# Performance work log

Measured on AMD Instinct MI355X. Metric: run time of the kernel, lower is better.

The kernel has to match this reference:

```python
import jax, jax.numpy as jnp
import numpy as np
from jax.ops import segment_sum

N_NODES = 50000


def gcn_conv(x, src, dst, W, b, n_nodes):
    # PyG GCNConv with default add_self_loops=True, normalize=True.
    # deg includes self-loops (weight 1 each).
    deg = segment_sum(jnp.ones_like(dst, dtype=x.dtype), dst, num_segments=n_nodes) + 1.0
    dinv = jax.lax.rsqrt(deg)  # [N]
    h = x @ W                  # [N, out]
    # messages over real edges: norm[src]*norm[dst]*h[src]
    msg = h[src] * (dinv[src] * dinv[dst])[:, None]   # [E, out]
    agg = segment_sum(msg, dst, num_segments=n_nodes)  # [N, out]
    # self-loop contribution: dinv[i]^2 * h[i]
    agg = agg + h * (dinv * dinv)[:, None]
    return agg + b


def setup_inputs() -> dict:
    key = jax.random.key(0)
    k1, k2, k3, k4 = jax.random.split(key, 4)
    N, E, d_in, d_hid, d_out = N_NODES, 800000, 128, 128, 64
    x = jax.random.normal(k1, (N, d_in), dtype=jnp.float32)
    edge_index = jax.random.randint(k2, (2, E), 0, N, dtype=jnp.int64)
    W1 = jax.random.normal(k3, (d_in, d_hid), dtype=jnp.float32) / np.sqrt(d_in)
    b1 = jnp.zeros((d_hid,), dtype=jnp.float32)
    W2 = jax.random.normal(k4, (d_hid, d_out), dtype=jnp.float32) / np.sqrt(d_hid)
    b2 = jnp.zeros((d_out,), dtype=jnp.float32)
    return {"x": x, "edge_index": edge_index, "W1": W1, "b1": b1, "W2": W2, "b2": b2}


def reference(x, edge_index, W1, b1, W2, b2):
    src, dst = edge_index[0], edge_index[1]
    h = gcn_conv(x, src, dst, W1, b1, N_NODES)
    h = jax.nn.relu(h)
    out = gcn_conv(h, src, dst, W2, b2, N_NODES)
    return out
```

## Files before the change

### kernel.cpp

```cpp
#include <hip/hip_runtime.h>
#include <hip/hip_bf16.h>


#define ELL_CAP 64
#define NPART 8

typedef __attribute__((ext_vector_type(8))) short short8;
typedef __attribute__((ext_vector_type(4))) float f32x4;

static __device__ __forceinline__ unsigned short f2bf(float f) {
    unsigned int u = __float_as_uint(f);
    u = (u + 0x7fff + ((u >> 16) & 1)) >> 16;
    return (unsigned short)u;
}
static __device__ __forceinline__ float2 bfunpack(unsigned int u) {
    return make_float2(__uint_as_float(u << 16),
                       __uint_as_float(u & 0xffff0000u));
}


__global__ void init_misc(const float* __restrict__ W1, const float* __restrict__ W2,
                          short* __restrict__ w1t, short* __restrict__ w2t,
                          int* __restrict__ cnt, int n)
{
    int i = blockIdx.x * blockDim.x + threadIdx.x;
    if (i < 128 * 128) {
        int k = i >> 7, nn = i & 127;
        w1t[nn * 128 + k] = (short)f2bf(W1[i]);
    } else if (i < 128 * 128 + 128 * 64) {
        int j = i - 128 * 128;
        int k = j >> 6, nn = j & 63;
        w2t[nn * 128 + k] = (short)f2bf(W2[j]);
    }
    if (i < n) cnt[i] = 0;
}


__global__ __launch_bounds__(256) void build_ell_part(
    const int* __restrict__ src, const int* __restrict__ dst,
    int* __restrict__ cnt, unsigned short* __restrict__ ell, int E, int partSize)
{
    const int part   = blockIdx.x & (NPART - 1);
    const int chunk  = blockIdx.x >> 3;
    const int nchunk = gridDim.x >> 3;
    const int lo = part * partSize, hi = lo + partSize;

    const int  E4  = E >> 2;
    const int  per = (E4 + nchunk - 1) / nchunk;
    const int  i1  = min((chunk + 1) * per, E4);
    const int4* __restrict__ d4p = (const int4*)dst;
    const int4* __restrict__ s4p = (const int4*)src;

    for (int i = chunk * per + threadIdx.x; i < i1; i += 256) {
        int4 d4 = d4p[i];
        int4 s4 = s4p[i];
        if (d4.x >= lo && d4.x < hi) {
            int p = atomicAdd(&cnt[d4.x], 1);
            if (p < ELL_CAP) ell[(size_t)d4.x * ELL_CAP + p] = (unsigned short)s4.x;
        }
        if (d4.y >= lo && d4.y < hi) {
            int p = atomicAdd(&cnt[d4.y], 1);
            if (p < ELL_CAP) ell[(size_t)d4.y * ELL_CAP + p] = (unsigned short)s4.y;
        }
        if (d4.z >= lo && d4.z < hi) {
            int p = atomicAdd(&cnt[d4.z], 1);
            if (p < ELL_CAP) ell[(size_t)d4.z * ELL_CAP + p] = (unsigned short)s4.z;
        }
        if (d4.w >= lo && d4.w < hi) {
            int p = atomicAdd(&cnt[d4.w], 1);
            if (p < ELL_CAP) ell[(size_t)d4.w * ELL_CAP + p] = (unsigned short)s4.w;
        }
    }
    if (chunk == 0) {
        for (int e = (E & ~3) + threadIdx.x; e < E; e += 256) {
            int d = dst[e];
            if (d >= lo && d < hi) {
                int p = atomicAdd(&cnt[d], 1);
                if (p < ELL_CAP) ell[(size_t)d * ELL_CAP + p] = (unsigned short)src[e];
            }
        }
    }
}


template<int NC, bool AF32>
__global__ __launch_bounds__(256) void gemm_mfma(
    const void* __restrict__ Av, const short* __restrict__ Bt,
    const int* __restrict__ cnt, unsigned short* __restrict__ Cb, int n)
{
    __shared__ short Bs[NC][136];
    const int tid = threadIdx.x;

    #pragma unroll
    for (int i = 0; i < NC / 16; ++i) {
        int idx = tid + i * 256;
        int nrow = idx >> 4;
        int kcol = (idx & 15) * 8;
        *(short8*)&Bs[nrow][kcol] = *(const short8*)(Bt + nrow * 128 + kcol);
    }
    __syncthreads();

    const int wave = tid >> 6, lane = tid & 63;
    const int row0 = blockIdx.x * 64 + wave * 16;
    if (row0 >= n) return;
    const int quad = lane >> 4, l16 = lane & 15;

    short8 af[4];
    if (AF32) {
        const float* arow = (const float*)Av + (size_t)(row0 + l16) * 128 + quad * 8;
        #pragma unroll
        for (int kk = 0; kk < 4; ++kk) {
            float4 u = *(const float4*)(arow + kk * 32);
            float4 v = *(const float4*)(arow + kk * 32 + 4);
            short8 f;
            f[0] = (short)f2bf(u.x); f[1] = (short)f2bf(u.y);
            f[2] = (short)f2bf(u.z); f[3] = (short)f2bf(u.w);
            f[4] = (short)f2bf(v.x); f[5] = (short)f2bf(v.y);
            f[6] = (short)f2bf(v.z); f[7] = (short)f2bf(v.w);
            af[kk] = f;
        }
    } else {
        const short* arow = (const short*)Av + (size_t)(row0 + l16) * 128 + quad * 8;
        #pragma unroll
        for (int kk = 0; kk < 4; ++kk)
            af[kk] = *(const short8*)(arow + kk * 32);
    }

    float dv[4];
    #pragma unroll
    for (int r = 0; r < 4; ++r)
        dv[r] = rsqrtf((float)cnt[row0 + quad * 4 + r] + 1.0f);

    #pragma unroll
    for (int t = 0; t < NC / 16; ++t) {
        f32x4 acc = {0.f, 0.f, 0.f, 0.f};
        #pragma unroll
        for (int kk = 0; kk < 4; ++kk) {
            short8 bfr = *(const short8*)&Bs[t * 16 + l16][kk * 32 + quad * 8];
            acc = __builtin_amdgcn_mfma_f32_16x16x32_bf16(af[kk], bfr, acc, 0, 0, 0);
        }
        #pragma unroll
        for (int r = 0; r < 4; ++r) {
            int gr = row0 + quad * 4 + r;
            Cb[(size_t)gr * NC + t * 16 + l16] = f2bf(acc[r] * dv[r]);
        }
    }
}


__global__ __launch_bounds__(256) void aggregate_l1(
    const unsigned int* __restrict__ hp, const unsigned short* __restrict__ ell,
    const int* __restrict__ cnt, const float* __restrict__ bias,
    unsigned int* __restrict__ z1b, int n)
{
    int node = blockIdx.x * 4 + (threadIdx.x >> 6);
    if (node >= n) return;
    int lane = threadIdx.x & 63;
    int deg = cnt[node];
    float d = rsqrtf((float)deg + 1.0f);
    if (deg > ELL_CAP) deg = ELL_CAP;
    const unsigned short* __restrict__ row = ell + (size_t)node * ELL_CAP;

    float2 acc = bfunpack(hp[(size_t)node * 64 + lane]);
    int e = 0;
    for (; e + 4 <= deg; e += 4) {
        uint2 w = *(const uint2*)&row[e];
        int s0 = w.x & 0xffff, s1 = w.x >> 16;
        int s2 = w.y & 0xffff, s3 = w.y >> 16;
        float2 v0 = bfunpack(hp[(size_t)s0 * 64 + lane]);
        float2 v1 = bfunpack(hp[(size_t)s1 * 64 + lane]);
        float2 v2 = bfunpack(hp[(size_t)s2 * 64 + lane]);
        float2 v3 = bfunpack(hp[(size_t)s3 * 64 + lane]);
        acc.x += (v0.x + v1.x) + (v2.x + v3.x);
        acc.y += (v0.y + v1.y) + (v2.y + v3.y);
    }
    for (; e < deg; ++e) {
        float2 v = bfunpack(hp[(size_t)row[e] * 64 + lane]);
        acc.x += v.x; acc.y += v.y;
    }
    float ox = fmaxf(fmaf(acc.x, d, bias[lane * 2]), 0.f);
    float oy = fmaxf(fmaf(acc.y, d, bias[lane * 2 + 1]), 0.f);
    z1b[(size_t)node * 64 + lane] =
        (unsigned int)f2bf(ox) | ((unsigned int)f2bf(oy) << 16);
}


__global__ __launch_bounds__(256) void aggregate_l2(
    const unsigned int* __restrict__ hp, const unsigned short* __restrict__ ell,
    const int* __restrict__ cnt, const float* __restrict__ bias,
    float* __restrict__ out, int n)
{
    int lane = threadIdx.x & 63;
    int half = lane >> 5, l32 = lane & 31;
    int node = blockIdx.x * 8 + (threadIdx.x >> 6) * 2 + half;
    if (node >= n) return;
    int deg = cnt[node];
    float d = rsqrtf((float)deg + 1.0f);
    if (deg > ELL_CAP) deg = ELL_CAP;
    const unsigned short* __restrict__ row = ell + (size_t)node * ELL_CAP;

    float2 acc = bfunpack(hp[(size_t)node * 32 + l32]);
    int e = 0;
    for (; e + 4 <= deg; e += 4) {
        uint2 w = *(const uint2*)&row[e];
        int s0 = w.x & 0xffff, s1 = w.x >> 16;
        int s2 = w.y & 0xffff, s3 = w.y >> 16;
        float2 v0 = bfunpack(hp[(size_t)s0 * 32 + l32]);
        float2 v1 = bfunpack(hp[(size_t)s1 * 32 + l32]);
        float2 v2 = bfunpack(hp[(size_t)s2 * 32 + l32]);
        float2 v3 = bfunpack(hp[(size_t)s3 * 32 + l32]);
        acc.x += (v0.x + v1.x) + (v2.x + v3.x);
        acc.y += (v0.y + v1.y) + (v2.y + v3.y);
    }
    for (; e < deg; ++e) {
        float2 v = bfunpack(hp[(size_t)row[e] * 32 + l32]);
        acc.x += v.x; acc.y += v.y;
    }
    float2 o;
    o.x = fmaf(acc.x, d, bias[l32 * 2]);
    o.y = fmaf(acc.y, d, bias[l32 * 2 + 1]);
    ((float2*)out)[(size_t)node * 32 + l32] = o;
}


extern "C" void kernel_launch(void* const* d_in, const int* in_sizes, int n_in,
                              void* d_out, int out_size, void* d_ws, size_t ws_size,
                              hipStream_t stream)
{
    const float* x  = (const float*)d_in[0];
    const int*   ei = (const int*)d_in[1];
    const float* W1 = (const float*)d_in[2];
    const float* b1 = (const float*)d_in[3];
    const float* W2 = (const float*)d_in[4];
    const float* b2 = (const float*)d_in[5];
    float* out = (float*)d_out;

    const int N = in_sizes[0] / 128;
    const int E = in_sizes[1] / 2;
    const int* src = ei;
    const int* dst = ei + E;
    const int partSize = (N + NPART - 1) / NPART;

    char* ws = (char*)d_ws;
    size_t off = 0;
    auto alloc = [&](size_t bytes) -> void* {
        void* p = ws + off;
        off += (bytes + 255) & ~(size_t)255;
        return p;
    };
    int*            cnt  = (int*)           alloc((size_t)N * 4);
    unsigned short* ell  = (unsigned short*)alloc((size_t)N * ELL_CAP * 2);
    short*          w1t  = (short*)         alloc((size_t)128 * 128 * 2);
    short*          w2t  = (short*)         alloc((size_t)64 * 128 * 2);
    unsigned short* h1b  = (unsigned short*)alloc((size_t)N * 128 * 2);
    unsigned int*   z1b  = (unsigned int*)  alloc((size_t)N * 64 * 4);
    unsigned short* h2b  = (unsigned short*)alloc((size_t)N * 64 * 2);

    init_misc<<<(N + 255) / 256, 256, 0, stream>>>(W1, W2, w1t, w2t, cnt, N);
    build_ell_part<<<256 * NPART, 256, 0, stream>>>(src, dst, cnt, ell, E, partSize);

    gemm_mfma<128, true><<<(N + 63) / 64, 256, 0, stream>>>(x, w1t, cnt, h1b, N);
    aggregate_l1<<<(N + 3) / 4, 256, 0, stream>>>((const unsigned int*)h1b, ell, cnt, b1, z1b, N);

    gemm_mfma<64, false><<<(N + 63) / 64, 256, 0, stream>>>(z1b, w2t, cnt, h2b, N);
    aggregate_l2<<<(N + 7) / 8, 256, 0, stream>>>((const unsigned int*)h2b, ell, cnt, b2, out, N);
}
```

Before: 197.4 us.

## Fuse ELL build with first GEMM and move source-degree scaling into aggregation

Merges the ELL graph construction, the W2 bf16 transpose and the first MFMA GEMM into one launch, with disjoint block ranges doing each job. The layer-1 GEMM can no longer scale rows by degree because counts are still being built, so aggregate_l1 now reads cnt for every neighbour and applies its rsqrt itself, broadcasting neighbour indices through readfirstlane. The cnt zeroing becomes a memset, and both aggregation loops unroll to 8 neighbours. This removes launches and overlaps the edge build with GEMM work, at the cost of extra per-edge cnt loads and rsqrt in layer 1.

```diff
diff --git a/kernel.cpp b/kernel.cpp
--- a/kernel.cpp
+++ b/kernel.cpp
@@ -4,6 +4,7 @@
 
 #define ELL_CAP 64
 #define NPART 8
+#define BCHUNK 128
 
 typedef __attribute__((ext_vector_type(8))) short short8;
 typedef __attribute__((ext_vector_type(4))) float f32x4;
@@ -19,95 +20,87 @@
 }
 
 
-__global__ void init_misc(const float* __restrict__ W1, const float* __restrict__ W2,
-                          short* __restrict__ w1t, short* __restrict__ w2t,
-                          int* __restrict__ cnt, int n)
-{
-    int i = blockIdx.x * blockDim.x + threadIdx.x;
-    if (i < 128 * 128) {
-        int k = i >> 7, nn = i & 127;
-        w1t[nn * 128 + k] = (short)f2bf(W1[i]);
-    } else if (i < 128 * 128 + 128 * 64) {
-        int j = i - 128 * 128;
-        int k = j >> 6, nn = j & 63;
-        w2t[nn * 128 + k] = (short)f2bf(W2[j]);
-    }
-    if (i < n) cnt[i] = 0;
-}
-
-
-__global__ __launch_bounds__(256) void build_ell_part(
+__global__ __launch_bounds__(256) void fused_b_g1(
+    const float* __restrict__ x, const float* __restrict__ W1,
+    const float* __restrict__ W2, short* __restrict__ w2t,
     const int* __restrict__ src, const int* __restrict__ dst,
-    int* __restrict__ cnt, unsigned short* __restrict__ ell, int E, int partSize)
-{
-    const int part   = blockIdx.x & (NPART - 1);
-    const int chunk  = blockIdx.x >> 3;
-    const int nchunk = gridDim.x >> 3;
-    const int lo = part * partSize, hi = lo + partSize;
-
-    const int  E4  = E >> 2;
-    const int  per = (E4 + nchunk - 1) / nchunk;
-    const int  i1  = min((chunk + 1) * per, E4);
-    const int4* __restrict__ d4p = (const int4*)dst;
-    const int4* __restrict__ s4p = (const int4*)src;
-
-    for (int i = chunk * per + threadIdx.x; i < i1; i += 256) {
-        int4 d4 = d4p[i];
-        int4 s4 = s4p[i];
-        if (d4.x >= lo && d4.x < hi) {
-            int p = atomicAdd(&cnt[d4.x], 1);
-            if (p < ELL_CAP) ell[(size_t)d4.x * ELL_CAP + p] = (unsigned short)s4.x;
-        }
-        if (d4.y >= lo && d4.y < hi) {
-            int p = atomicAdd(&cnt[d4.y], 1);
-            if (p < ELL_CAP) ell[(size_t)d4.y * ELL_CAP + p] = (unsigned short)s4.y;
-        }
-        if (d4.z >= lo && d4.z < hi) {
-            int p = atomicAdd(&cnt[d4.z], 1);
-            if (p < ELL_CAP) ell[(size_t)d4.z * ELL_CAP + p] = (unsigned short)s4.z;
-        }
-        if (d4.w >= lo && d4.w < hi) {
-            int p = atomicAdd(&cnt[d4.w], 1);
-            if (p < ELL_CAP) ell[(size_t)d4.w * ELL_CAP + p] = (unsigned short)s4.w;
-        }
-    }
-    if (chunk == 0) {
-        for (int e = (E & ~3) + threadIdx.x; e < E; e += 256) {
-            int d = dst[e];
-            if (d >= lo && d < hi) {
-                int p = atomicAdd(&cnt[d], 1);
-                if (p < ELL_CAP) ell[(size_t)d * ELL_CAP + p] = (unsigned short)src[e];
-            }
-        }
-    }
-}
-
-
-template<int NC, bool AF32>
-__global__ __launch_bounds__(256) void gemm_mfma(
-    const void* __restrict__ Av, const short* __restrict__ Bt,
-    const int* __restrict__ cnt, unsigned short* __restrict__ Cb, int n)
-{
-    __shared__ short Bs[NC][136];
+    int* __restrict__ cnt, unsigned short* __restrict__ ell,
+    unsigned short* __restrict__ h1b,
+    int n, int E, int partSize, int nGemm)
+{
+    __shared__ short Bs[128][136];
+    const int bid = blockIdx.x;
     const int tid = threadIdx.x;
 
-    #pragma unroll
-    for (int i = 0; i < NC / 16; ++i) {
-        int idx = tid + i * 256;
-        int nrow = idx >> 4;
-        int kcol = (idx & 15) * 8;
-        *(short8*)&Bs[nrow][kcol] = *(const short8*)(Bt + nrow * 128 + kcol);
+    if (bid >= nGemm) {
+        if (bid == nGemm + NPART * BCHUNK) {
+            for (int i = tid; i < 128 * 64; i += 256) {
+                int k = i >> 6, nn = i & 63;
+                w2t[nn * 128 + k] = (short)f2bf(W2[i]);
+            }
+            return;
+        }
+        const int part  = bid & (NPART - 1);
+        const int rel   = bid - nGemm;
+        const int chunk = rel >> 3;
+        const int lo = part * partSize, hi = lo + partSize;
+        const int E4  = E >> 2;
+        const int per = (E4 + BCHUNK - 1) / BCHUNK;
+        const int i1  = min((chunk + 1) * per, E4);
+        const int4* __restrict__ d4p = (const int4*)dst;
+        const int4* __restrict__ s4p = (const int4*)src;
+        for (int i = chunk * per + tid; i < i1; i += 256) {
+            int4 d4 = d4p[i];
+            int4 s4 = s4p[i];
+            if (d4.x >= lo && d4.x < hi) {
+                int p = atomicAdd(&cnt[d4.x], 1);
+                if (p < ELL_CAP) ell[(size_t)d4.x * ELL_CAP + p] = (unsigned short)s4.x;
+            }
+            if (d4.y >= lo && d4.y < hi) {
+                int p = atomicAdd(&cnt[d4.y], 1);
+                if (p < ELL_CAP) ell[(size_t)d4.y * ELL_CAP + p] = (unsigned short)s4.y;
+            }
+            if (d4.z >= lo && d4.z < hi) {
+                int p = atomicAdd(&cnt[d4.z], 1);
+                if (p < ELL_CAP) ell[(size_t)d4.z * ELL_CAP + p] = (unsigned short)s4.z;
+            }
+            if (d4.w >= lo && d4.w < hi) {
+                int p = atomicAdd(&cnt[d4.w], 1);
+                if (p < ELL_CAP) ell[(size_t)d4.w * ELL_CAP + p] = (unsigned short)s4.w;
+            }
+        }
+        if (chunk == 0) {
+            for (int e = (E & ~3) + tid; e < E; e += 256) {
+                int d = dst[e];
+                if (d >= lo && d < hi) {
+                    int p = atomicAdd(&cnt[d], 1);
+                    if (p < ELL_CAP) ell[(size_t)d * ELL_CAP + p] = (unsigned short)src[e];
+                }
+            }
+        }
+        return;
+    }
+
+    #pragma unroll
+    for (int i = 0; i < 16; ++i) {
+        int idx = (tid + i * 256) * 4;
+        int k = idx >> 7, nn = idx & 127;
+        float4 u = *(const float4*)(W1 + idx);
+        Bs[nn + 0][k] = (short)f2bf(u.x);
+        Bs[nn + 1][k] = (short)f2bf(u.y);
+        Bs[nn + 2][k] = (short)f2bf(u.z);
+        Bs[nn + 3][k] = (short)f2bf(u.w);
     }
     __syncthreads();
 
     const int wave = tid >> 6, lane = tid & 63;
-    const int row0 = blockIdx.x * 64 + wave * 16;
+    const int row0 = bid * 64 + wave * 16;
     if (row0 >= n) return;
     const int quad = lane >> 4, l16 = lane & 15;
 
     short8 af[4];
-    if (AF32) {
-        const float* arow = (const float*)Av + (size_t)(row0 + l16) * 128 + quad * 8;
+    {
+        const float* arow = x + (size_t)(row0 + l16) * 128 + quad * 8;
         #pragma unroll
         for (int kk = 0; kk < 4; ++kk) {
             float4 u = *(const float4*)(arow + kk * 32);
@@ -119,8 +112,50 @@
             f[6] = (short)f2bf(v.z); f[7] = (short)f2bf(v.w);
             af[kk] = f;
         }
-    } else {
-        const short* arow = (const short*)Av + (size_t)(row0 + l16) * 128 + quad * 8;
+    }
+
+    #pragma unroll
+    for (int t = 0; t < 8; ++t) {
+        f32x4 acc = {0.f, 0.f, 0.f, 0.f};
+        #pragma unroll
+        for (int kk = 0; kk < 4; ++kk) {
+            short8 bfr = *(const short8*)&Bs[t * 16 + l16][kk * 32 + quad * 8];
+            acc = __builtin_amdgcn_mfma_f32_16x16x32_bf16(af[kk], bfr, acc, 0, 0, 0);
+        }
+        #pragma unroll
+        for (int r = 0; r < 4; ++r) {
+            int gr = row0 + quad * 4 + r;
+            h1b[(size_t)gr * 128 + t * 16 + l16] = f2bf(acc[r]);
+        }
+    }
+}
+
+
+template<int NC>
+__global__ __launch_bounds__(256) void gemm_mfma(
+    const short* __restrict__ A, const short* __restrict__ Bt,
+    const int* __restrict__ cnt, unsigned short* __restrict__ Cb, int n)
+{
+    __shared__ short Bs[NC][136];
+    const int tid = threadIdx.x;
+
+    #pragma unroll
+    for (int i = 0; i < NC / 16; ++i) {
+        int idx = tid + i * 256;
+        int nrow = idx >> 4;
+        int kcol = (idx & 15) * 8;
+        *(short8*)&Bs[nrow][kcol] = *(const short8*)(Bt + nrow * 128 + kcol);
+    }
+    __syncthreads();
+
+    const int wave = tid >> 6, lane = tid & 63;
+    const int row0 = blockIdx.x * 64 + wave * 16;
+    if (row0 >= n) return;
+    const int quad = lane >> 4, l16 = lane & 15;
+
+    short8 af[4];
+    {
+        const short* arow = A + (size_t)(row0 + l16) * 128 + quad * 8;
         #pragma unroll
         for (int kk = 0; kk < 4; ++kk)
             af[kk] = *(const short8*)(arow + kk * 32);
@@ -161,22 +196,46 @@
     if (deg > ELL_CAP) deg = ELL_CAP;
     const unsigned short* __restrict__ row = ell + (size_t)node * ELL_CAP;
 
-    float2 acc = bfunpack(hp[(size_t)node * 64 + lane]);
+    float2 vs = bfunpack(hp[(size_t)node * 64 + lane]);
+    float2 acc = make_float2(vs.x * d, vs.y * d);
     int e = 0;
-    for (; e + 4 <= deg; e += 4) {
-        uint2 w = *(const uint2*)&row[e];
-        int s0 = w.x & 0xffff, s1 = w.x >> 16;
-        int s2 = w.y & 0xffff, s3 = w.y >> 16;
+    for (; e + 8 <= deg; e += 8) {
+        uint4 w = *(const uint4*)&row[e];
+        int s0 = __builtin_amdgcn_readfirstlane((int)(w.x & 0xffff));
+        int s1 = __builtin_amdgcn_readfirstlane((int)(w.x >> 16));
+        int s2 = __builtin_amdgcn_readfirstlane((int)(w.y & 0xffff));
+        int s3 = __builtin_amdgcn_readfirstlane((int)(w.y >> 16));
+        int s4 = __builtin_amdgcn_readfirstlane((int)(w.z & 0xffff));
+        int s5 = __builtin_amdgcn_readfirstlane((int)(w.z >> 16));
+        int s6 = __builtin_amdgcn_readfirstlane((int)(w.w & 0xffff));
+        int s7 = __builtin_amdgcn_readfirstlane((int)(w.w >> 16));
+        float q0 = rsqrtf((float)cnt[s0] + 1.0f);
+        float q1 = rsqrtf((float)cnt[s1] + 1.0f);
+        float q2 = rsqrtf((float)cnt[s2] + 1.0f);
+        float q3 = rsqrtf((float)cnt[s3] + 1.0f);
+        float q4 = rsqrtf((float)cnt[s4] + 1.0f);
+        float q5 = rsqrtf((float)cnt[s5] + 1.0f);
+        float q6 = rsqrtf((float)cnt[s6] + 1.0f);
+        float q7 = rsqrtf((float)cnt[s7] + 1.0f);
         float2 v0 = bfunpack(hp[(size_t)s0 * 64 + lane]);
         float2 v1 = bfunpack(hp[(size_t)s1 * 64 + lane]);
         float2 v2 = bfunpack(hp[(size_t)s2 * 64 + lane]);
         float2 v3 = bfunpack(hp[(size_t)s3 * 64 + lane]);
-        acc.x += (v0.x + v1.x) + (v2.x + v3.x);
-        acc.y += (v0.y + v1.y) + (v2.y + v3.y);
+        float2 v4 = bfunpack(hp[(size_t)s4 * 64 + lane]);
+        float2 v5 = bfunpack(hp[(size_t)s5 * 64 + lane]);
+        float2 v6 = bfunpack(hp[(size_t)s6 * 64 + lane]);
+        float2 v7 = bfunpack(hp[(size_t)s7 * 64 + lane]);
+        acc.x += (fmaf(v0.x, q0, v1.x * q1) + fmaf(v2.x, q2, v3.x * q3))
+               + (fmaf(v4.x, q4, v5.x * q5) + fmaf(v6.x, q6, v7.x * q7));
+        acc.y += (fmaf(v0.y, q0, v1.y * q1) + fmaf(v2.y, q2, v3.y * q3))
+               + (fmaf(v4.y, q4, v5.y * q5) + fmaf(v6.y, q6, v7.y * q7));
     }
     for (; e < deg; ++e) {
-        float2 v = bfunpack(hp[(size_t)row[e] * 64 + lane]);
-        acc.x += v.x; acc.y += v.y;
+        int s = __builtin_amdgcn_readfirstlane((int)row[e]);
+        float q = rsqrtf((float)cnt[s] + 1.0f);
+        float2 v = bfunpack(hp[(size_t)s * 64 + lane]);
+        acc.x = fmaf(v.x, q, acc.x);
+        acc.y = fmaf(v.y, q, acc.y);
     }
     float ox = fmaxf(fmaf(acc.x, d, bias[lane * 2]), 0.f);
     float oy = fmaxf(fmaf(acc.y, d, bias[lane * 2 + 1]), 0.f);
@@ -201,6 +260,23 @@
 
     float2 acc = bfunpack(hp[(size_t)node * 32 + l32]);
     int e = 0;
+    for (; e + 8 <= deg; e += 8) {
+        uint4 w = *(const uint4*)&row[e];
+        int s0 = w.x & 0xffff, s1 = w.x >> 16;
+        int s2 = w.y & 0xffff, s3 = w.y >> 16;
+        int s4 = w.z & 0xffff, s5 = w.z >> 16;
+        int s6 = w.w & 0xffff, s7 = w.w >> 16;
+        float2 v0 = bfunpack(hp[(size_t)s0 * 32 + l32]);
+        float2 v1 = bfunpack(hp[(size_t)s1 * 32 + l32]);
+        float2 v2 = bfunpack(hp[(size_t)s2 * 32 + l32]);
+        float2 v3 = bfunpack(hp[(size_t)s3 * 32 + l32]);
+        float2 v4 = bfunpack(hp[(size_t)s4 * 32 + l32]);
+        float2 v5 = bfunpack(hp[(size_t)s5 * 32 + l32]);
+        float2 v6 = bfunpack(hp[(size_t)s6 * 32 + l32]);
+        float2 v7 = bfunpack(hp[(size_t)s7 * 32 + l32]);
+        acc.x += ((v0.x + v1.x) + (v2.x + v3.x)) + ((v4.x + v5.x) + (v6.x + v7.x));
+        acc.y += ((v0.y + v1.y) + (v2.y + v3.y)) + ((v4.y + v5.y) + (v6.y + v7.y));
+    }
     for (; e + 4 <= deg; e += 4) {
         uint2 w = *(const uint2*)&row[e];
         int s0 = w.x & 0xffff, s1 = w.x >> 16;
@@ -240,6 +316,7 @@
     const int* src = ei;
     const int* dst = ei + E;
     const int partSize = (N + NPART - 1) / NPART;
+    const int nGemm = (N + 63) / 64;
 
     char* ws = (char*)d_ws;
     size_t off = 0;
@@ -250,18 +327,22 @@
     };
     int*            cnt  = (int*)           alloc((size_t)N * 4);
     unsigned short* ell  = (unsigned short*)alloc((size_t)N * ELL_CAP * 2);
-    short*          w1t  = (short*)         alloc((size_t)128 * 128 * 2);
     short*          w2t  = (short*)         alloc((size_t)64 * 128 * 2);
     unsigned short* h1b  = (unsigned short*)alloc((size_t)N * 128 * 2);
     unsigned int*   z1b  = (unsigned int*)  alloc((size_t)N * 64 * 4);
     unsigned short* h2b  = (unsigned short*)alloc((size_t)N * 64 * 2);
 
-    init_misc<<<(N + 255) / 256, 256, 0, stream>>>(W1, W2, w1t, w2t, cnt, N);
-    build_ell_part<<<256 * NPART, 256, 0, stream>>>(src, dst, cnt, ell, E, partSize);
-
-    gemm_mfma<128, true><<<(N + 63) / 64, 256, 0, stream>>>(x, w1t, cnt, h1b, N);
-    aggregate_l1<<<(N + 3) / 4, 256, 0, stream>>>((const unsigned int*)h1b, ell, cnt, b1, z1b, N);
-
-    gemm_mfma<64, false><<<(N + 63) / 64, 256, 0, stream>>>(z1b, w2t, cnt, h2b, N);
-    aggregate_l2<<<(N + 7) / 8, 256, 0, stream>>>((const unsigned int*)h2b, ell, cnt, b2, out, N);
-}
+    hipMemsetAsync(cnt, 0, (size_t)N * 4, stream);
+
+    fused_b_g1<<<nGemm + NPART * BCHUNK + 1, 256, 0, stream>>>(
+        x, W1, W2, w2t, src, dst, cnt, ell, h1b, N, E, partSize, nGemm);
+
+    aggregate_l1<<<(N + 3) / 4, 256, 0, stream>>>(
+        (const unsigned int*)h1b, ell, cnt, b1, z1b, N);
+
+    gemm_mfma<64><<<(N + 63) / 64, 256, 0, stream>>>(
+        (const short*)z1b, w2t, cnt, h2b, N);
+
+    aggregate_l2<<<(N + 7) / 8, 256, 0, stream>>>(
+        (const unsigned int*)h2b, ell, cnt, b2, out, N);
+}
```

Result: no change. 195.0 us (-1.2%).

## Store features in 32-column chunk-major layout and aggregate chunk by chunk

Applied to the files above, without the earlier changes.

The GEMM now writes its bf16 outputs in a chunk-major layout: column blocks of 32 are stored contiguously across all nodes. Aggregation runs as separate launches per chunk, four for layer 1 and two for layer 2, so each pass gathers from a smaller working set (N×64 bytes) that fits better in L2/MALL. The goal is a higher cache hit rate on random neighbor gathers. The cost is re-reading the ELL index array once per chunk, extra launches, and only 64-byte gathers per neighbor. The inner gather loop is also unrolled to 8 neighbors.

```diff
diff --git a/kernel.cpp b/kernel.cpp
--- a/kernel.cpp
+++ b/kernel.cpp
@@ -120,10 +120,10 @@
             af[kk] = f;
         }
     } else {
-        const short* arow = (const short*)Av + (size_t)(row0 + l16) * 128 + quad * 8;
         #pragma unroll
         for (int kk = 0; kk < 4; ++kk)
-            af[kk] = *(const short8*)(arow + kk * 32);
+            af[kk] = *(const short8*)((const short*)Av + (size_t)kk * n * 32
+                                      + (size_t)(row0 + l16) * 32 + quad * 8);
     }
 
     float dv[4];
@@ -142,84 +142,77 @@
         #pragma unroll
         for (int r = 0; r < 4; ++r) {
             int gr = row0 + quad * 4 + r;
-            Cb[(size_t)gr * NC + t * 16 + l16] = f2bf(acc[r] * dv[r]);
-        }
-    }
-}
-
-
-__global__ __launch_bounds__(256) void aggregate_l1(
-    const unsigned int* __restrict__ hp, const unsigned short* __restrict__ ell,
-    const int* __restrict__ cnt, const float* __restrict__ bias,
-    unsigned int* __restrict__ z1b, int n)
-{
-    int node = blockIdx.x * 4 + (threadIdx.x >> 6);
+            Cb[(size_t)(t >> 1) * n * 32 + (size_t)gr * 32 + (t & 1) * 16 + l16]
+                = f2bf(acc[r] * dv[r]);
+        }
+    }
+}
+
+
+template<bool FINAL>
+__global__ __launch_bounds__(256) void aggregate_chunk(
+    const unsigned int* __restrict__ hc,
+    const unsigned short* __restrict__ ell,
+    const int* __restrict__ cnt, const float* __restrict__ biasc,
+    unsigned int* __restrict__ zc,
+    float* __restrict__ outc,
+    int n)
+{
+    const int q = threadIdx.x >> 4, l16 = threadIdx.x & 15;
+    const int node = blockIdx.x * 16 + q;
     if (node >= n) return;
-    int lane = threadIdx.x & 63;
     int deg = cnt[node];
-    float d = rsqrtf((float)deg + 1.0f);
+    const float d = rsqrtf((float)deg + 1.0f);
     if (deg > ELL_CAP) deg = ELL_CAP;
     const unsigned short* __restrict__ row = ell + (size_t)node * ELL_CAP;
 
-    float2 acc = bfunpack(hp[(size_t)node * 64 + lane]);
+    float2 acc = bfunpack(hc[(size_t)node * 16 + l16]);
     int e = 0;
+    for (; e + 8 <= deg; e += 8) {
+        uint4 w = *(const uint4*)&row[e];
+        int s0 = w.x & 0xffff, s1 = w.x >> 16;
+        int s2 = w.y & 0xffff, s3 = w.y >> 16;
+        int s4 = w.z & 0xffff, s5 = w.z >> 16;
+        int s6 = w.w & 0xffff, s7 = w.w >> 16;
+        float2 v0 = bfunpack(hc[(size_t)s0 * 16 + l16]);
+        float2 v1 = bfunpack(hc[(size_t)s1 * 16 + l16]);
+        float2 v2 = bfunpack(hc[(size_t)s2 * 16 + l16]);
+        float2 v3 = bfunpack(hc[(size_t)s3 * 16 + l16]);
+        float2 v4 = bfunpack(hc[(size_t)s4 * 16 + l16]);
+        float2 v5 = bfunpack(hc[(size_t)s5 * 16 + l16]);
+        float2 v6 = bfunpack(hc[(size_t)s6 * 16 + l16]);
+        float2 v7 = bfunpack(hc[(size_t)s7 * 16 + l16]);
+        acc.x += ((v0.x + v1.x) + (v2.x + v3.x)) + ((v4.x + v5.x) + (v6.x + v7.x));
+        acc.y += ((v0.y + v1.y) + (v2.y + v3.y)) + ((v4.y + v5.y) + (v6.y + v7.y));
+    }
     for (; e + 4 <= deg; e += 4) {
         uint2 w = *(const uint2*)&row[e];
         int s0 = w.x & 0xffff, s1 = w.x >> 16;
         int s2 = w.y & 0xffff, s3 = w.y >> 16;
-        float2 v0 = bfunpack(hp[(size_t)s0 * 64 + lane]);
-        float2 v1 = bfunpack(hp[(size_t)s1 * 64 + lane]);
-        float2 v2 = bfunpack(hp[(size_t)s2 * 64 + lane]);
-        float2 v3 = bfunpack(hp[(size_t)s3 * 64 + lane]);
+        float2 v0 = bfunpack(hc[(size_t)s0 * 16 + l16]);
+        float2 v1 = bfunpack(hc[(size_t)s1 * 16 + l16]);
+        float2 v2 = bfunpack(hc[(size_t)s2 * 16 + l16]);
+        float2 v3 = bfunpack(hc[(size_t)s3 * 16 + l16]);
         acc.x += (v0.x + v1.x) + (v2.x + v3.x);
         acc.y += (v0.y + v1.y) + (v2.y + v3.y);
     }
     for (; e < deg; ++e) {
-        float2 v = bfunpack(hp[(size_t)row[e] * 64 + lane]);
+        float2 v = bfunpack(hc[(size_t)row[e] * 16 + l16]);
         acc.x += v.x; acc.y += v.y;
     }
-    float ox = fmaxf(fmaf(acc.x, d, bias[lane * 2]), 0.f);
-    float oy = fmaxf(fmaf(acc.y, d, bias[lane * 2 + 1]), 0.f);
-    z1b[(size_t)node * 64 + lane] =
-        (unsigned int)f2bf(ox) | ((unsigned int)f2bf(oy) << 16);
-}
-
-
-__global__ __launch_bounds__(256) void aggregate_l2(
-    const unsigned int* __restrict__ hp, const unsigned short* __restrict__ ell,
-    const int* __restrict__ cnt, const float* __restrict__ bias,
-    float* __restrict__ out, int n)
-{
-    int lane = threadIdx.x & 63;
-    int half = lane >> 5, l32 = lane & 31;
-    int node = blockIdx.x * 8 + (threadIdx.x >> 6) * 2 + half;
-    if (node >= n) return;
-    int deg = cnt[node];
-    float d = rsqrtf((float)deg + 1.0f);
-    if (deg > ELL_CAP) deg = ELL_CAP;
-    const unsigned short* __restrict__ row = ell + (size_t)node * ELL_CAP;
-
-    float2 acc = bfunpack(hp[(size_t)node * 32 + l32]);
-    int e = 0;
-    for (; e + 4 <= deg; e += 4) {
-        uint2 w = *(const uint2*)&row[e];
-        int s0 = w.x & 0xffff, s1 = w.x >> 16;
-        int s2 = w.y & 0xffff, s3 = w.y >> 16;
-        float2 v0 = bfunpack(hp[(size_t)s0 * 32 + l32]);
-        float2 v1 = bfunpack(hp[(size_t)s1 * 32 + l32]);
-        float2 v2 = bfunpack(hp[(size_t)s2 * 32 + l32]);
-        float2 v3 = bfunpack(hp[(size_t)s3 * 32 + l32]);
-        acc.x += (v0.x + v1.x) + (v2.x + v3.x);
-        acc.y += (v0.y + v1.y) + (v2.y + v3.y);
-    }
-    for (; e < deg; ++e) {
-        float2 v = bfunpack(hp[(size_t)row[e] * 32 + l32]);
-        acc.x += v.x; acc.y += v.y;
-    }
-    float2 o;
-    o.x = fmaf(acc.x, d, bias[l32 * 2]);
-    o.y = fmaf(acc.y, d, bias[l32 * 2 + 1]);
-    ((float2*)out)[(size_t)node * 32 + l32] = o;
+
+    float2 b = *(const float2*)(biasc + l16 * 2);
+    if (FINAL) {
+        float2 o;
+        o.x = fmaf(acc.x, d, b.x);
+        o.y = fmaf(acc.y, d, b.y);
+        ((float2*)outc)[(size_t)node * 32 + l16] = o;
+    } else {
+        float ox = fmaxf(fmaf(acc.x, d, b.x), 0.f);
+        float oy = fmaxf(fmaf(acc.y, d, b.y), 0.f);
+        zc[(size_t)node * 16 + l16] =
+            (unsigned int)f2bf(ox) | ((unsigned int)f2bf(oy) << 16);
+    }
 }
 
 
@@ -252,16 +245,25 @@
     unsigned short* ell  = (unsigned short*)alloc((size_t)N * ELL_CAP * 2);
     short*          w1t  = (short*)         alloc((size_t)128 * 128 * 2);
     short*          w2t  = (short*)         alloc((size_t)64 * 128 * 2);
-    unsigned short* h1b  = (unsigned short*)alloc((size_t)N * 128 * 2);
-    unsigned int*   z1b  = (unsigned int*)  alloc((size_t)N * 64 * 4);
-    unsigned short* h2b  = (unsigned short*)alloc((size_t)N * 64 * 2);
+    unsigned short* h1c  = (unsigned short*)alloc((size_t)N * 128 * 2);
+    unsigned int*   z1c  = (unsigned int*)  alloc((size_t)N * 64 * 4);
+    unsigned short* h2c  = (unsigned short*)alloc((size_t)N * 64 * 2);
 
     init_misc<<<(N + 255) / 256, 256, 0, stream>>>(W1, W2, w1t, w2t, cnt, N);
     build_ell_part<<<256 * NPART, 256, 0, stream>>>(src, dst, cnt, ell, E, partSize);
 
-    gemm_mfma<128, true><<<(N + 63) / 64, 256, 0, stream>>>(x, w1t, cnt, h1b, N);
-    aggregate_l1<<<(N + 3) / 4, 256, 0, stream>>>((const unsigned int*)h1b, ell, cnt, b1, z1b, N);
-
-    gemm_mfma<64, false><<<(N + 63) / 64, 256, 0, stream>>>(z1b, w2t, cnt, h2b, N);
-    aggregate_l2<<<(N + 7) / 8, 256, 0, stream>>>((const unsigned int*)h2b, ell, cnt, b2, out, N);
-}
+    gemm_mfma<128, true><<<(N + 63) / 64, 256, 0, stream>>>(x, w1t, cnt, h1c, N);
+    const int aggBlocks = (N + 15) / 16;
+    for (int c = 0; c < 4; ++c) {
+        aggregate_chunk<false><<<aggBlocks, 256, 0, stream>>>(
+            (const unsigned int*)h1c + (size_t)c * N * 16, ell, cnt,
+            b1 + c * 32, z1c + (size_t)c * N * 16, nullptr, N);
+    }
+
+    gemm_mfma<64, false><<<(N + 63) / 64, 256, 0, stream>>>(z1c, w2t, cnt, h2c, N);
+    for (int c = 0; c < 2; ++c) {
+        aggregate_chunk<true><<<aggBlocks, 256, 0, stream>>>(
+            (const unsigned int*)h2c + (size_t)c * N * 16, ell, cnt,
+            b2 + c * 32, nullptr, out + c * 32, N);
+    }
+}
```

After: 211.5 us. 7.2% more time.

## Gather multiple neighbor rows per wave with 16-byte loads in aggregation

Applied to the files above, without the earlier changes.

Both aggregation kernels now split a wavefront into groups that each gather a different neighbor row with a 16-byte vector load, then combine the partial sums with cross-lane shuffles. Previously the whole wavefront read one row per step with 4-byte loads. The goal is fewer, wider memory transactions and more gathers in flight per wave. In exchange there is padding work for degrees that are not a multiple of the group count, extra shuffles, and more lanes left idle when writing results. The count-zeroing step also moves from the weight-conversion kernel to hipMemsetAsync.

```diff
diff --git a/kernel.cpp b/kernel.cpp
--- a/kernel.cpp
+++ b/kernel.cpp
@@ -19,9 +19,8 @@
 }
 
 
-__global__ void init_misc(const float* __restrict__ W1, const float* __restrict__ W2,
-                          short* __restrict__ w1t, short* __restrict__ w2t,
-                          int* __restrict__ cnt, int n)
+__global__ void convert_weights(const float* __restrict__ W1, const float* __restrict__ W2,
+                                short* __restrict__ w1t, short* __restrict__ w2t)
 {
     int i = blockIdx.x * blockDim.x + threadIdx.x;
     if (i < 128 * 128) {
@@ -32,7 +31,6 @@
         int k = j >> 6, nn = j & 63;
         w2t[nn * 128 + k] = (short)f2bf(W2[j]);
     }
-    if (i < n) cnt[i] = 0;
 }
 
 
@@ -149,77 +147,133 @@
 
 
 __global__ __launch_bounds__(256) void aggregate_l1(
-    const unsigned int* __restrict__ hp, const unsigned short* __restrict__ ell,
+    const unsigned short* __restrict__ hb,
+    const unsigned short* __restrict__ ell,
     const int* __restrict__ cnt, const float* __restrict__ bias,
     unsigned int* __restrict__ z1b, int n)
 {
-    int node = blockIdx.x * 4 + (threadIdx.x >> 6);
+    const int node = blockIdx.x * 4 + (threadIdx.x >> 6);
     if (node >= n) return;
-    int lane = threadIdx.x & 63;
+    const int lane = threadIdx.x & 63;
+    const int quad = lane >> 4, l16 = lane & 15;
+
     int deg = cnt[node];
-    float d = rsqrtf((float)deg + 1.0f);
+    const float d = rsqrtf((float)deg + 1.0f);
     if (deg > ELL_CAP) deg = ELL_CAP;
     const unsigned short* __restrict__ row = ell + (size_t)node * ELL_CAP;
 
-    float2 acc = bfunpack(hp[(size_t)node * 64 + lane]);
-    int e = 0;
-    for (; e + 4 <= deg; e += 4) {
-        uint2 w = *(const uint2*)&row[e];
-        int s0 = w.x & 0xffff, s1 = w.x >> 16;
-        int s2 = w.y & 0xffff, s3 = w.y >> 16;
-        float2 v0 = bfunpack(hp[(size_t)s0 * 64 + lane]);
-        float2 v1 = bfunpack(hp[(size_t)s1 * 64 + lane]);
-        float2 v2 = bfunpack(hp[(size_t)s2 * 64 + lane]);
-        float2 v3 = bfunpack(hp[(size_t)s3 * 64 + lane]);
-        acc.x += (v0.x + v1.x) + (v2.x + v3.x);
-        acc.y += (v0.y + v1.y) + (v2.y + v3.y);
-    }
-    for (; e < deg; ++e) {
-        float2 v = bfunpack(hp[(size_t)row[e] * 64 + lane]);
-        acc.x += v.x; acc.y += v.y;
-    }
-    float ox = fmaxf(fmaf(acc.x, d, bias[lane * 2]), 0.f);
-    float oy = fmaxf(fmaf(acc.y, d, bias[lane * 2 + 1]), 0.f);
-    z1b[(size_t)node * 64 + lane] =
-        (unsigned int)f2bf(ox) | ((unsigned int)f2bf(oy) << 16);
+    float acc[8];
+    {
+        uint4 v = *(const uint4*)(hb + (size_t)node * 128 + l16 * 8);
+        bool val = (quad == 0);
+        #pragma unroll
+        for (int j = 0; j < 4; ++j) {
+            float2 f = bfunpack(((const unsigned int*)&v)[j]);
+            acc[2 * j]     = val ? f.x : 0.f;
+            acc[2 * j + 1] = val ? f.y : 0.f;
+        }
+    }
+    const int degR = (deg + 3) & ~3;
+    #pragma unroll 2
+    for (int e = 0; e < degR; e += 4) {
+        unsigned int w0 = *(const unsigned int*)&row[e];
+        unsigned int w1 = *(const unsigned int*)&row[e + 2];
+        unsigned int hw = (quad & 2) ? w1 : w0;
+        int s = (quad & 1) ? (int)(hw >> 16) : (int)(hw & 0xffff);
+        s = min(s, n - 1);
+        uint4 v = *(const uint4*)(hb + (size_t)s * 128 + l16 * 8);
+        bool val = (e + quad < deg);
+        #pragma unroll
+        for (int j = 0; j < 4; ++j) {
+            float2 f = bfunpack(((const unsigned int*)&v)[j]);
+            acc[2 * j]     += val ? f.x : 0.f;
+            acc[2 * j + 1] += val ? f.y : 0.f;
+        }
+    }
+    #pragma unroll
+    for (int j = 0; j < 8; ++j) {
+        acc[j] += __shfl_xor(acc[j], 16);
+        acc[j] += __shfl_xor(acc[j], 32);
+    }
+    if (quad == 0) {
+        unsigned int ow[4];
+        #pragma unroll
+        for (int j = 0; j < 4; ++j) {
+            float bx = bias[l16 * 8 + 2 * j];
+            float by = bias[l16 * 8 + 2 * j + 1];
+            float ox = fmaxf(fmaf(acc[2 * j],     d, bx), 0.f);
+            float oy = fmaxf(fmaf(acc[2 * j + 1], d, by), 0.f);
+            ow[j] = (unsigned int)f2bf(ox) | ((unsigned int)f2bf(oy) << 16);
+        }
+        *(uint4*)&z1b[(size_t)node * 64 + l16 * 4] = *(const uint4*)ow;
+    }
 }
 
 
 __global__ __launch_bounds__(256) void aggregate_l2(
-    const unsigned int* __restrict__ hp, const unsigned short* __restrict__ ell,
+    const unsigned short* __restrict__ hb,
+    const unsigned short* __restrict__ ell,
     const int* __restrict__ cnt, const float* __restrict__ bias,
     float* __restrict__ out, int n)
 {
-    int lane = threadIdx.x & 63;
-    int half = lane >> 5, l32 = lane & 31;
-    int node = blockIdx.x * 8 + (threadIdx.x >> 6) * 2 + half;
+    const int node = blockIdx.x * 4 + (threadIdx.x >> 6);
     if (node >= n) return;
+    const int lane = threadIdx.x & 63;
+    const int oct = lane >> 3, l8 = lane & 7;
+
     int deg = cnt[node];
-    float d = rsqrtf((float)deg + 1.0f);
+    const float d = rsqrtf((float)deg + 1.0f);
     if (deg > ELL_CAP) deg = ELL_CAP;
     const unsigned short* __restrict__ row = ell + (size_t)node * ELL_CAP;
 
-    float2 acc = bfunpack(hp[(size_t)node * 32 + l32]);
-    int e = 0;
-    for (; e + 4 <= deg; e += 4) {
-        uint2 w = *(const uint2*)&row[e];
-        int s0 = w.x & 0xffff, s1 = w.x >> 16;
-        int s2 = w.y & 0xffff, s3 = w.y >> 16;
-        float2 v0 = bfunpack(hp[(size_t)s0 * 32 + l32]);
-        float2 v1 = bfunpack(hp[(size_t)s1 * 32 + l32]);
-        float2 v2 = bfunpack(hp[(size_t)s2 * 32 + l32]);
-        float2 v3 = bfunpack(hp[(size_t)s3 * 32 + l32]);
-        acc.x += (v0.x + v1.x) + (v2.x + v3.x);
-        acc.y += (v0.y + v1.y) + (v2.y + v3.y);
-    }
-    for (; e < deg; ++e) {
-        float2 v = bfunpack(hp[(size_t)row[e] * 32 + l32]);
-        acc.x += v.x; acc.y += v.y;
-    }
-    float2 o;
-    o.x = fmaf(acc.x, d, bias[l32 * 2]);
-    o.y = fmaf(acc.y, d, bias[l32 * 2 + 1]);
-    ((float2*)out)[(size_t)node * 32 + l32] = o;
+    float acc[8];
+    {
+        uint4 v = *(const uint4*)(hb + (size_t)node * 64 + l8 * 8);
+        bool val = (oct == 0);
+        #pragma unroll
+        for (int j = 0; j < 4; ++j) {
+            float2 f = bfunpack(((const unsigned int*)&v)[j]);
+            acc[2 * j]     = val ? f.x : 0.f;
+            acc[2 * j + 1] = val ? f.y : 0.f;
+        }
+    }
+    const int degR = (deg + 7) & ~7;
+    #pragma unroll 2
+    for (int e = 0; e < degR; e += 8) {
+        uint4 w = *(const uint4*)&row[e];
+        unsigned int pw = (oct & 4) ? ((oct & 2) ? w.w : w.z)
+                                    : ((oct & 2) ? w.y : w.x);
+        int s = (oct & 1) ? (int)(pw >> 16) : (int)(pw & 0xffff);
+        s = min(s, n - 1);
+        uint4 v = *(const uint4*)(hb + (size_t)s * 64 + l8 * 8);
+        bool val = (e + oct < deg);
+        #pragma unroll
+        for (int j = 0; j < 4; ++j) {
+            float2 f = bfunpack(((const unsigned int*)&v)[j]);
+            acc[2 * j]     += val ? f.x : 0.f;
+            acc[2 * j + 1] += val ? f.y : 0.f;
+        }
+    }
+    #pragma unroll
+    for (int j = 0; j < 8; ++j) {
+        acc[j] += __shfl_xor(acc[j], 8);
+        acc[j] += __shfl_xor(acc[j], 16);
+        acc[j] += __shfl_xor(acc[j], 32);
+    }
+    if (oct == 0) {
+        float* op = out + (size_t)node * 64 + l8 * 8;
+        float4 o0, o1;
+        o0.x = fmaf(acc[0], d, bias[l8 * 8 + 0]);
+        o0.y = fmaf(acc[1], d, bias[l8 * 8 + 1]);
+        o0.z = fmaf(acc[2], d, bias[l8 * 8 + 2]);
+        o0.w = fmaf(acc[3], d, bias[l8 * 8 + 3]);
+        o1.x = fmaf(acc[4], d, bias[l8 * 8 + 4]);
+        o1.y = fmaf(acc[5], d, bias[l8 * 8 + 5]);
+        o1.z = fmaf(acc[6], d, bias[l8 * 8 + 6]);
+        o1.w = fmaf(acc[7], d, bias[l8 * 8 + 7]);
+        *(float4*)(op)     = o0;
+        *(float4*)(op + 4) = o1;
+    }
 }
 
 
@@ -256,12 +310,13 @@
     unsigned int*   z1b  = (unsigned int*)  alloc((size_t)N * 64 * 4);
     unsigned short* h2b  = (unsigned short*)alloc((size_t)N * 64 * 2);
 
-    init_misc<<<(N + 255) / 256, 256, 0, stream>>>(W1, W2, w1t, w2t, cnt, N);
+    hipMemsetAsync(cnt, 0, (size_t)N * 4, stream);
+    convert_weights<<<(128 * 192 + 255) / 256, 256, 0, stream>>>(W1, W2, w1t, w2t);
     build_ell_part<<<256 * NPART, 256, 0, stream>>>(src, dst, cnt, ell, E, partSize);
 
     gemm_mfma<128, true><<<(N + 63) / 64, 256, 0, stream>>>(x, w1t, cnt, h1b, N);
-    aggregate_l1<<<(N + 3) / 4, 256, 0, stream>>>((const unsigned int*)h1b, ell, cnt, b1, z1b, N);
+    aggregate_l1<<<(N + 3) / 4, 256, 0, stream>>>(h1b, ell, cnt, b1, z1b, N);
 
     gemm_mfma<64, false><<<(N + 63) / 64, 256, 0, stream>>>(z1b, w2t, cnt, h2b, N);
-    aggregate_l2<<<(N + 7) / 8, 256, 0, stream>>>((const unsigned int*)h2b, ell, cnt, b2, out, N);
-}
+    aggregate_l2<<<(N + 3) / 4, 256, 0, stream>>>(h2b, ell, cnt, b2, out, N);
+}
```

Measured after the change: 198.6 us. No clear change (+0.6%).
